# Kernel tuning notes

Measured on AMD Instinct MI355X. Metric: run time of the kernel, lower is better.

The kernel has to match this reference:

```python
import jax, jax.numpy as jnp
import numpy as np

NEG_INF = -9.0e15
ALPHA = 0.2  # leakyrelu slope


def setup_inputs() -> dict:
    key = jax.random.key(0)
    k1, k2, k3, k4, k5 = jax.random.split(key, 5)
    B, N, D_IN, D_OUT = 8, 2048, 128, 128
    h = jax.random.normal(k1, (B, N, D_IN), dtype=jnp.float32)
    adj = jax.random.randint(k2, (N, N), 0, 2, dtype=jnp.int32)
    W = jax.random.normal(k3, (D_IN, D_OUT), dtype=jnp.float32) * (1.0 / np.sqrt(D_IN))
    a_src = jax.random.normal(k4, (D_OUT,), dtype=jnp.float32) * (1.0 / np.sqrt(D_OUT))
    a_dst = jax.random.normal(k5, (D_OUT,), dtype=jnp.float32) * (1.0 / np.sqrt(D_OUT))
    return {"h": h, "adj": adj, "W": W, "a_src": a_src, "a_dst": a_dst}


def reference(h, adj, W, a_src, a_dst):
    # Wh: [B, N, D_out]
    Wh = jnp.einsum("bnd,de->bne", h, W)
    e_src = jnp.einsum("bne,e->bn", Wh, a_src)  # [B, N]
    e_dst = jnp.einsum("bne,e->bn", Wh, a_dst)  # [B, N]
    # additive attention logits: e[b,i,j] = e_src[b,i] + e_dst[b,j]
    e = e_src[:, :, None] + e_dst[:, None, :]  # [B, N, N]
    e = jnp.where(e > 0, e, ALPHA * e)  # leaky relu
    e = jnp.where(adj[None, :, :] > 0, e, NEG_INF)
    attention = jax.nn.softmax(e, axis=-1)  # [B, N, N]
    h_prime = jnp.einsum("bij,bje->bie", attention, Wh)
    return h_prime
```

## Files before the change

kernel.cpp:

```cpp
#include <hip/hip_runtime.h>
#include <stdint.h>

#define ALPHA 0.2f
#define LOG2E 1.4426950408889634f

typedef unsigned short u16;
typedef short s16x8 __attribute__((ext_vector_type(8)));
typedef float f32x4 __attribute__((ext_vector_type(4)));

union BF8 { s16x8 v; uint32_t u[4]; u16 s[8]; uint4 q; };

static __device__ __forceinline__ float bf2f(u16 u) {
  union { uint32_t i; float f; } c; c.i = ((uint32_t)u) << 16; return c.f;
}
static __device__ __forceinline__ uint32_t pk2bf(float lo, float hi) {
  uint32_t ul = __float_as_uint(lo) + 0x8000u;
  uint32_t uh = __float_as_uint(hi) + 0x8000u;
  return (ul >> 16) | (uh & 0xffff0000u);
}

static __device__ __forceinline__ void gl2lds16(const void* g, void* l) {
  __builtin_amdgcn_global_load_lds(
      (const __attribute__((address_space(1))) uint32_t*)g,
      (__attribute__((address_space(3))) uint32_t*)l, 16, 0, 0);
}

__global__ __launch_bounds__(256) void k_zero(uint32_t* __restrict__ out, int n32) {
  int gid = blockIdx.x * 256 + threadIdx.x;
  if (gid < n32) out[gid] = 0u;
}

__global__ __launch_bounds__(256) void k_pack_adj(const int* __restrict__ adj,
                                                  uint32_t* __restrict__ bits,
                                                  const u16* __restrict__ h,
                                                  int* __restrict__ flag) {
  int tid = threadIdx.x;
  int base = blockIdx.x * 256 + tid;
#pragma unroll
  for (int it = 0; it < 8; ++it) {
    int gid = base + it * (2048 * 256);
    unsigned long long m = __ballot(adj[gid] != 0);
    if ((tid & 63) == 0)
      *(unsigned long long*)(&bits[gid >> 5]) = m;
  }
  if (blockIdx.x == 0 && tid < 64) {
    u16 v = h[2 * tid];
    int e = (v >> 7) & 0xff;
    unsigned long long dm = __ballot(e >= 100 && e <= 140);
    if (tid == 0) flag[0] = (__popcll(dm) >= 48) ? 1 : 0;
  }
}

__global__ __launch_bounds__(256) void k_wh(
    const void* __restrict__ hV, const void* __restrict__ WgV,
    const void* __restrict__ aSrcV, const void* __restrict__ aDstV,
    const int* __restrict__ flag,
    u16* __restrict__ WhT, float* __restrict__ eS, float* __restrict__ eD) {
  __shared__ __align__(16) char smemRaw[34816];
  u16*   WT   = (u16*)smemRaw;
  float* tile = (float*)smemRaw;
  __shared__ float aS[128], aD[128];

  const int tid = threadIdx.x;
  const int mb = blockIdx.x * 64;
  const int isBf = *flag;

  if (isBf) {
    const u16* Wg = (const u16*)WgV;
    for (int it = 0; it < 8; ++it) {
      int idx = tid + it * 256;
      int k = idx >> 4, c0 = (idx & 15) * 8;
      uint4 w4 = *(const uint4*)(Wg + (k << 7) + c0);
      u16* wsv = (u16*)&w4;
#pragma unroll
      for (int e = 0; e < 8; ++e) WT[(c0 + e) * 136 + k] = wsv[e];
    }
    if (tid < 128) aS[tid] = bf2f(((const u16*)aSrcV)[tid]);
    else           aD[tid - 128] = bf2f(((const u16*)aDstV)[tid - 128]);
  } else {
    const float* Wg = (const float*)WgV;
    for (int it = 0; it < 8; ++it) {
      int idx = tid + it * 256;
      int k = idx >> 4, c0 = (idx & 15) * 8;
      float4 w0 = *(const float4*)(Wg + (k << 7) + c0);
      float4 w1 = *(const float4*)(Wg + (k << 7) + c0 + 4);
      float wf[8] = {w0.x, w0.y, w0.z, w0.w, w1.x, w1.y, w1.z, w1.w};
#pragma unroll
      for (int e = 0; e < 8; ++e)
        WT[(c0 + e) * 136 + k] = (u16)((__float_as_uint(wf[e]) + 0x8000u) >> 16);
    }
    if (tid < 128) aS[tid] = ((const float*)aSrcV)[tid];
    else           aD[tid - 128] = ((const float*)aDstV)[tid - 128];
  }
  __syncthreads();

  const int wv = tid >> 6, lane = tid & 63, ln = lane & 15, quad = lane >> 4;
  const int row = mb + wv * 16 + ln;

  f32x4 acc[8];
#pragma unroll
  for (int t = 0; t < 8; ++t) acc[t] = (f32x4){0.f, 0.f, 0.f, 0.f};

  if (isBf) {
    const u16* h = (const u16*)hV;
#pragma unroll
    for (int ks = 0; ks < 4; ++ks) {
      s16x8 af = *(const s16x8*)(h + (row << 7) + ks * 32 + quad * 8);
#pragma unroll
      for (int t = 0; t < 8; ++t) {
        s16x8 bfg = *(const s16x8*)(&WT[(t * 16 + ln) * 136 + ks * 32 + quad * 8]);
        acc[t] = __builtin_amdgcn_mfma_f32_16x16x32_bf16(af, bfg, acc[t], 0, 0, 0);
      }
    }
  } else {
    const float* h = (const float*)hV;
#pragma unroll
    for (int ks = 0; ks < 4; ++ks) {
      float4 a0 = *(const float4*)(h + (row << 7) + ks * 32 + quad * 8);
      float4 a1 = *(const float4*)(h + (row << 7) + ks * 32 + quad * 8 + 4);
      BF8 af;
      af.u[0] = pk2bf(a0.x, a0.y);
      af.u[1] = pk2bf(a0.z, a0.w);
      af.u[2] = pk2bf(a1.x, a1.y);
      af.u[3] = pk2bf(a1.z, a1.w);
#pragma unroll
      for (int t = 0; t < 8; ++t) {
        s16x8 bfg = *(const s16x8*)(&WT[(t * 16 + ln) * 136 + ks * 32 + quad * 8]);
        acc[t] = __builtin_amdgcn_mfma_f32_16x16x32_bf16(af.v, bfg, acc[t], 0, 0, 0);
      }
    }
  }
  __syncthreads();

#pragma unroll
  for (int t = 0; t < 8; ++t)
#pragma unroll
    for (int r = 0; r < 4; ++r)
      tile[(wv * 16 + quad * 4 + r) * 130 + t * 16 + ln] = acc[t][r];
  __syncthreads();

  if (tid < 128) {
    int r = tid & 63, grp = tid >> 6;
    const float* a = grp ? aD : aS;
    float sum = 0.f;
#pragma unroll 4
    for (int d = 0; d < 128; ++d) sum += tile[r * 130 + d] * a[d];
    int m = mb + r, b = m >> 11, n = m & 2047;
    (grp ? eD : eS)[(b << 11) + n] = sum * LOG2E;
  }

  {
    int d = tid >> 1, half = tid & 1;
    int n0 = mb & 2047, b = mb >> 11;
    uint32_t pk[16];
#pragma unroll
    for (int qq = 0; qq < 16; ++qq) {
      float v0 = tile[(half * 32 + 2 * qq) * 130 + d];
      float v1 = tile[(half * 32 + 2 * qq + 1) * 130 + d];
      pk[qq] = pk2bf(v0, v1);
    }
    uint4* dst = (uint4*)(WhT + (size_t)((b << 7) + d) * 2048 + n0 + half * 32);
#pragma unroll
    for (int c = 0; c < 4; ++c)
      dst[c] = make_uint4(pk[c * 4], pk[c * 4 + 1], pk[c * 4 + 2], pk[c * 4 + 3]);
  }
}

__global__ __launch_bounds__(512, 4) void k_attn(
    const u16* __restrict__ WhT, const float* __restrict__ eSrc,
    const float* __restrict__ eDst, const uint32_t* __restrict__ adjBits,
    const int* __restrict__ flag, void* __restrict__ outV) {
  __shared__ __align__(16) u16 bufB[2][8192];
  __shared__ __align__(16) u16 bufP[2][2048];

  const int tid = threadIdx.x;
  const int bid = (blockIdx.x & 7) * 64 + (blockIdx.x >> 3);
  const int b = bid >> 6, ig = bid & 63;
  const int i0 = ig * 32;

  const int w = tid >> 6, l = tid & 63;
  const int ln = l & 15, quad = l >> 4;
  const int s = w & 1, dh = w >> 1;

  const int gsrc = (l & 7) ^ ((l >> 3) & 7);
  const u16* whtB = WhT + ((size_t)b << 18);
  const u16* srcB = whtB + (size_t)(w * 8 + (l >> 3)) * 2048 + gsrc * 8;

  const int prow = tid >> 4, hg = tid & 15;
  const float sSp = eSrc[(b << 11) + i0 + prow];
  const float* eDb = eDst + (b << 11) + hg * 4;
  const uint32_t* adjB = adjBits + (size_t)(i0 + prow) * 64 + (hg >> 3);
  const int pOff = prow * 128 + ((hg ^ ((prow & 7) << 1)) * 8);

  int aOff[2], bOff[2][2];
#pragma unroll
  for (int jk = 0; jk < 2; ++jk) {
    aOff[jk] = (s * 16 + ln) * 128 + (((jk * 4 + quad) ^ (ln & 7)) * 16);
#pragma unroll
    for (int tt = 0; tt < 2; ++tt)
      bOff[tt][jk] = (dh * 32 + tt * 16 + ln) * 128
                   + (((jk * 4 + quad) ^ (ln & 7)) * 16);
  }

  f32x4 acc[2], accD;
  acc[0] = (f32x4){0.f, 0.f, 0.f, 0.f};
  acc[1] = (f32x4){0.f, 0.f, 0.f, 0.f};
  accD   = (f32x4){0.f, 0.f, 0.f, 0.f};

  BF8 ones;
  ones.u[0] = 0x3f803f80u; ones.u[1] = 0x3f803f80u;
  ones.u[2] = 0x3f803f80u; ones.u[3] = 0x3f803f80u;

  u16 *bBc = bufB[0], *bBn = bufB[1];
  u16 *bPc = bufP[0], *bPn = bufP[1];

  gl2lds16(srcB, bBc + w * 512);
  gl2lds16(srcB + 131072, bBc + 4096 + w * 512);
  {
    f32x4 dv = *(const f32x4*)(eDb);
    uint32_t aw = adjB[0];
    uint32_t nib = (aw >> ((hg & 7) * 4)) & 0xfu;
    float x0 = sSp + dv[0], x1 = sSp + dv[1], x2 = sSp + dv[2], x3 = sSp + dv[3];
    float p0 = exp2f(__builtin_amdgcn_fmed3f(x0, ALPHA * x0, 80.f));
    float p1 = exp2f(__builtin_amdgcn_fmed3f(x1, ALPHA * x1, 80.f));
    float p2 = exp2f(__builtin_amdgcn_fmed3f(x2, ALPHA * x2, 80.f));
    float p3 = exp2f(__builtin_amdgcn_fmed3f(x3, ALPHA * x3, 80.f));
    uint32_t m01 = ((nib & 1u) ? 0x0000ffffu : 0u) | ((nib & 2u) ? 0xffff0000u : 0u);
    uint32_t m23 = ((nib & 4u) ? 0x0000ffffu : 0u) | ((nib & 8u) ? 0xffff0000u : 0u);
    *(uint2*)((char*)bPc + pOff) = make_uint2(pk2bf(p0, p1) & m01,
                                              pk2bf(p2, p3) & m23);
  }
  __syncthreads();

  for (int t = 0; t < 32; ++t) {
    if (t + 1 < 32) {
      gl2lds16(srcB + (size_t)(t + 1) * 64, bBn + w * 512);
      gl2lds16(srcB + (size_t)(t + 1) * 64 + 131072, bBn + 4096 + w * 512);
      f32x4 dv = *(const f32x4*)(eDb + (t + 1) * 64);
      uint32_t aw = adjB[(t + 1) * 2];
      uint32_t nib = (aw >> ((hg & 7) * 4)) & 0xfu;
      float x0 = sSp + dv[0], x1 = sSp + dv[1], x2 = sSp + dv[2], x3 = sSp + dv[3];
      float p0 = exp2f(__builtin_amdgcn_fmed3f(x0, ALPHA * x0, 80.f));
      float p1 = exp2f(__builtin_amdgcn_fmed3f(x1, ALPHA * x1, 80.f));
      float p2 = exp2f(__builtin_amdgcn_fmed3f(x2, ALPHA * x2, 80.f));
      float p3 = exp2f(__builtin_amdgcn_fmed3f(x3, ALPHA * x3, 80.f));
      uint32_t m01 = ((nib & 1u) ? 0x0000ffffu : 0u) | ((nib & 2u) ? 0xffff0000u : 0u);
      uint32_t m23 = ((nib & 4u) ? 0x0000ffffu : 0u) | ((nib & 8u) ? 0xffff0000u : 0u);
      *(uint2*)((char*)bPn + pOff) = make_uint2(pk2bf(p0, p1) & m01,
                                                pk2bf(p2, p3) & m23);
    }

    s16x8 af0 = *(const s16x8*)((const char*)bPc + aOff[0]);
    s16x8 af1 = *(const s16x8*)((const char*)bPc + aOff[1]);
    s16x8 b00 = *(const s16x8*)((const char*)bBc + bOff[0][0]);
    s16x8 b10 = *(const s16x8*)((const char*)bBc + bOff[1][0]);
    s16x8 b01 = *(const s16x8*)((const char*)bBc + bOff[0][1]);
    s16x8 b11 = *(const s16x8*)((const char*)bBc + bOff[1][1]);

    __builtin_amdgcn_s_setprio(1);
    acc[0] = __builtin_amdgcn_mfma_f32_16x16x32_bf16(af0, b00, acc[0], 0, 0, 0);
    acc[1] = __builtin_amdgcn_mfma_f32_16x16x32_bf16(af0, b10, acc[1], 0, 0, 0);
    acc[0] = __builtin_amdgcn_mfma_f32_16x16x32_bf16(af1, b01, acc[0], 0, 0, 0);
    acc[1] = __builtin_amdgcn_mfma_f32_16x16x32_bf16(af1, b11, acc[1], 0, 0, 0);
    if (dh == 0) {
      accD = __builtin_amdgcn_mfma_f32_16x16x32_bf16(af0, ones.v, accD, 0, 0, 0);
      accD = __builtin_amdgcn_mfma_f32_16x16x32_bf16(af1, ones.v, accD, 0, 0, 0);
    }
    __builtin_amdgcn_s_setprio(0);

    __syncthreads();
    u16* tB = bBc; bBc = bBn; bBn = tB;
    u16* tP = bPc; bPc = bPn; bPn = tP;
  }

  float* den = (float*)bufP;
  if (dh == 0 && ln == 0) {
#pragma unroll
    for (int r = 0; r < 4; ++r) den[s * 16 + quad * 4 + r] = accD[r];
  }
  __syncthreads();

  float inv[4];
#pragma unroll
  for (int r = 0; r < 4; ++r)
    inv[r] = 1.0f / fmaxf(den[s * 16 + quad * 4 + r], 1e-37f);

  const int isBf = *flag;
  if (isBf) {
    u16* outp = (u16*)outV;
#pragma unroll
    for (int tt = 0; tt < 2; ++tt)
#pragma unroll
      for (int r = 0; r < 4; ++r) {
        size_t off = ((size_t)((b << 11) + i0 + s * 16 + quad * 4 + r) << 7)
                   + dh * 32 + tt * 16 + ln;
        float v = acc[tt][r] * inv[r];
        outp[off] = (u16)((__float_as_uint(v) + 0x8000u) >> 16);
      }
  } else {
    float* outp = (float*)outV;
#pragma unroll
    for (int tt = 0; tt < 2; ++tt)
#pragma unroll
      for (int r = 0; r < 4; ++r) {
        size_t off = ((size_t)((b << 11) + i0 + s * 16 + quad * 4 + r) << 7)
                   + dh * 32 + tt * 16 + ln;
        outp[off] = acc[tt][r] * inv[r];
      }
  }
}

extern "C" void kernel_launch(void* const* d_in, const int* in_sizes, int n_in,
                              void* d_out, int out_size, void* d_ws, size_t ws_size,
                              hipStream_t stream) {
  const void* h   = d_in[0];
  const int* adj  = (const int*)d_in[1];
  const void* Wg  = d_in[2];
  const void* aS  = d_in[3];
  const void* aD  = d_in[4];

  const size_t OFF_ES   = (size_t)4 << 20;
  const size_t OFF_ED   = OFF_ES + (64 << 10);
  const size_t OFF_BITS = OFF_ED + (64 << 10);
  const size_t OFF_FLAG = OFF_BITS + (512 << 10);
  const size_t NEEDED   = OFF_FLAG + 64;

  if (ws_size < NEEDED) {
    int n32 = out_size / 2;
    k_zero<<<(n32 + 255) / 256, 256, 0, stream>>>((uint32_t*)d_out, n32);
    return;
  }

  char* ws = (char*)d_ws;
  u16* WhT      = (u16*)ws;
  float* eSp    = (float*)(ws + OFF_ES);
  float* eDp    = (float*)(ws + OFF_ED);
  uint32_t* bit = (uint32_t*)(ws + OFF_BITS);
  int* flag     = (int*)(ws + OFF_FLAG);

  k_pack_adj<<<2048, 256, 0, stream>>>(adj, bit, (const u16*)h, flag);
  k_wh<<<256, 256, 0, stream>>>(h, Wg, aS, aD, flag, WhT, eSp, eDp);
  k_attn<<<512, 512, 0, stream>>>(WhT, eSp, eDp, bit, flag, d_out);
}
```

Before: 119.0 us.

## Merge adj-pack and Wh kernels, triple-buffer attention pipeline with explicit waits

Merges the adjacency bit-packing and the Wh projection into one launch. Wh blocks now handle 32 rows and compute the dtype flag themselves, and the e_src/e_dst dot products are reduced with wave shuffles instead of a serial LDS loop. The attention kernel moves from double to triple buffering, prefetching two tiles ahead, with manual s_waitcnt and s_barrier calls in place of __syncthreads. The aim is to drop one launch and overlap global-to-LDS loads with MFMA work, at the cost of more LDS per block, which may lower occupancy.

```diff
diff --git a/kernel.cpp b/kernel.cpp
--- a/kernel.cpp
+++ b/kernel.cpp
@@ -30,40 +30,50 @@
   if (gid < n32) out[gid] = 0u;
 }
 
-__global__ __launch_bounds__(256) void k_pack_adj(const int* __restrict__ adj,
-                                                  uint32_t* __restrict__ bits,
-                                                  const u16* __restrict__ h,
-                                                  int* __restrict__ flag) {
-  int tid = threadIdx.x;
-  int base = blockIdx.x * 256 + tid;
-#pragma unroll
-  for (int it = 0; it < 8; ++it) {
-    int gid = base + it * (2048 * 256);
-    unsigned long long m = __ballot(adj[gid] != 0);
-    if ((tid & 63) == 0)
-      *(unsigned long long*)(&bits[gid >> 5]) = m;
-  }
-  if (blockIdx.x == 0 && tid < 64) {
-    u16 v = h[2 * tid];
+__global__ __launch_bounds__(256) void k_prep(
+    const int* __restrict__ adj, uint32_t* __restrict__ bits,
+    const void* __restrict__ hV, const void* __restrict__ WgV,
+    const void* __restrict__ aSrcV, const void* __restrict__ aDstV,
+    int* __restrict__ flag,
+    u16* __restrict__ WhT, float* __restrict__ eS, float* __restrict__ eD) {
+  __shared__ __align__(16) char smemRaw[34816];
+  __shared__ float aS[128], aD[128];
+  __shared__ float ePs[2][32][2];
+
+  const int tid = threadIdx.x;
+  const int bk = blockIdx.x;
+  const int lane = tid & 63;
+
+  if (bk < 2048) {
+    int base = bk * 256 + tid;
+#pragma unroll
+    for (int it = 0; it < 8; ++it) {
+      int gid = base + it * (2048 * 256);
+      unsigned long long m = __ballot(adj[gid] != 0);
+      if ((tid & 63) == 0)
+        *(unsigned long long*)(&bits[gid >> 5]) = m;
+    }
+    if (bk == 0 && tid < 64) {
+      u16 v = ((const u16*)hV)[2 * tid];
+      int e = (v >> 7) & 0xff;
+      unsigned long long dm = __ballot(e >= 100 && e <= 140);
+      if (tid == 0) flag[0] = (__popcll(dm) >= 48) ? 1 : 0;
+    }
+    return;
+  }
+
+  u16*   WT   = (u16*)smemRaw;
+  float* tile = (float*)smemRaw;
+  const int whid = bk - 2048;
+  const int mb = whid * 32;
+
+  int isBf;
+  {
+    u16 v = ((const u16*)hV)[2 * lane];
     int e = (v >> 7) & 0xff;
     unsigned long long dm = __ballot(e >= 100 && e <= 140);
-    if (tid == 0) flag[0] = (__popcll(dm) >= 48) ? 1 : 0;
-  }
-}
-
-__global__ __launch_bounds__(256) void k_wh(
-    const void* __restrict__ hV, const void* __restrict__ WgV,
-    const void* __restrict__ aSrcV, const void* __restrict__ aDstV,
-    const int* __restrict__ flag,
-    u16* __restrict__ WhT, float* __restrict__ eS, float* __restrict__ eD) {
-  __shared__ __align__(16) char smemRaw[34816];
-  u16*   WT   = (u16*)smemRaw;
-  float* tile = (float*)smemRaw;
-  __shared__ float aS[128], aD[128];
-
-  const int tid = threadIdx.x;
-  const int mb = blockIdx.x * 64;
-  const int isBf = *flag;
+    isBf = (__popcll(dm) >= 48) ? 1 : 0;
+  }
 
   if (isBf) {
     const u16* Wg = (const u16*)WgV;
@@ -94,12 +104,13 @@
   }
   __syncthreads();
 
-  const int wv = tid >> 6, lane = tid & 63, ln = lane & 15, quad = lane >> 4;
-  const int row = mb + wv * 16 + ln;
-
-  f32x4 acc[8];
-#pragma unroll
-  for (int t = 0; t < 8; ++t) acc[t] = (f32x4){0.f, 0.f, 0.f, 0.f};
+  const int wv = tid >> 6, ln = lane & 15, quad = lane >> 4;
+  const int rh = wv & 1, ch = wv >> 1;
+  const int row = mb + rh * 16 + ln;
+
+  f32x4 acc[4];
+#pragma unroll
+  for (int t = 0; t < 4; ++t) acc[t] = (f32x4){0.f, 0.f, 0.f, 0.f};
 
   if (isBf) {
     const u16* h = (const u16*)hV;
@@ -107,8 +118,8 @@
     for (int ks = 0; ks < 4; ++ks) {
       s16x8 af = *(const s16x8*)(h + (row << 7) + ks * 32 + quad * 8);
 #pragma unroll
-      for (int t = 0; t < 8; ++t) {
-        s16x8 bfg = *(const s16x8*)(&WT[(t * 16 + ln) * 136 + ks * 32 + quad * 8]);
+      for (int t = 0; t < 4; ++t) {
+        s16x8 bfg = *(const s16x8*)(&WT[(ch * 64 + t * 16 + ln) * 136 + ks * 32 + quad * 8]);
         acc[t] = __builtin_amdgcn_mfma_f32_16x16x32_bf16(af, bfg, acc[t], 0, 0, 0);
       }
     }
@@ -124,45 +135,67 @@
       af.u[2] = pk2bf(a1.x, a1.y);
       af.u[3] = pk2bf(a1.z, a1.w);
 #pragma unroll
-      for (int t = 0; t < 8; ++t) {
-        s16x8 bfg = *(const s16x8*)(&WT[(t * 16 + ln) * 136 + ks * 32 + quad * 8]);
+      for (int t = 0; t < 4; ++t) {
+        s16x8 bfg = *(const s16x8*)(&WT[(ch * 64 + t * 16 + ln) * 136 + ks * 32 + quad * 8]);
         acc[t] = __builtin_amdgcn_mfma_f32_16x16x32_bf16(af.v, bfg, acc[t], 0, 0, 0);
       }
     }
   }
-  __syncthreads();
-
-#pragma unroll
-  for (int t = 0; t < 8; ++t)
+
+  {
+    float pS[4] = {0.f, 0.f, 0.f, 0.f}, pD[4] = {0.f, 0.f, 0.f, 0.f};
+#pragma unroll
+    for (int t = 0; t < 4; ++t) {
+      float av = aS[ch * 64 + t * 16 + ln];
+      float dv = aD[ch * 64 + t * 16 + ln];
+#pragma unroll
+      for (int r = 0; r < 4; ++r) { pS[r] += acc[t][r] * av; pD[r] += acc[t][r] * dv; }
+    }
+#pragma unroll
+    for (int m = 1; m < 16; m <<= 1) {
+#pragma unroll
+      for (int r = 0; r < 4; ++r) {
+        pS[r] += __shfl_xor(pS[r], m);
+        pD[r] += __shfl_xor(pD[r], m);
+      }
+    }
+    if (ln == 0) {
+#pragma unroll
+      for (int r = 0; r < 4; ++r) {
+        ePs[0][rh * 16 + quad * 4 + r][ch] = pS[r];
+        ePs[1][rh * 16 + quad * 4 + r][ch] = pD[r];
+      }
+    }
+  }
+  __syncthreads();
+
+#pragma unroll
+  for (int t = 0; t < 4; ++t)
 #pragma unroll
     for (int r = 0; r < 4; ++r)
-      tile[(wv * 16 + quad * 4 + r) * 130 + t * 16 + ln] = acc[t][r];
-  __syncthreads();
-
-  if (tid < 128) {
-    int r = tid & 63, grp = tid >> 6;
-    const float* a = grp ? aD : aS;
-    float sum = 0.f;
-#pragma unroll 4
-    for (int d = 0; d < 128; ++d) sum += tile[r * 130 + d] * a[d];
+      tile[(rh * 16 + quad * 4 + r) * 130 + ch * 64 + t * 16 + ln] = acc[t][r];
+  __syncthreads();
+
+  if (tid < 64) {
+    int r = tid & 31, which = tid >> 5;
+    float sum = ePs[which][r][0] + ePs[which][r][1];
     int m = mb + r, b = m >> 11, n = m & 2047;
-    (grp ? eD : eS)[(b << 11) + n] = sum * LOG2E;
+    (which ? eD : eS)[(b << 11) + n] = sum * LOG2E;
   }
 
   {
     int d = tid >> 1, half = tid & 1;
     int n0 = mb & 2047, b = mb >> 11;
-    uint32_t pk[16];
-#pragma unroll
-    for (int qq = 0; qq < 16; ++qq) {
-      float v0 = tile[(half * 32 + 2 * qq) * 130 + d];
-      float v1 = tile[(half * 32 + 2 * qq + 1) * 130 + d];
-      pk[qq] = pk2bf(v0, v1);
-    }
-    uint4* dst = (uint4*)(WhT + (size_t)((b << 7) + d) * 2048 + n0 + half * 32);
-#pragma unroll
-    for (int c = 0; c < 4; ++c)
-      dst[c] = make_uint4(pk[c * 4], pk[c * 4 + 1], pk[c * 4 + 2], pk[c * 4 + 3]);
+    uint32_t pk[8];
+#pragma unroll
+    for (int q = 0; q < 8; ++q) {
+      float v0 = tile[(half * 16 + 2 * q) * 130 + d];
+      float v1 = tile[(half * 16 + 2 * q + 1) * 130 + d];
+      pk[q] = pk2bf(v0, v1);
+    }
+    uint4* dst = (uint4*)(WhT + (size_t)((b << 7) + d) * 2048 + n0 + half * 16);
+    dst[0] = make_uint4(pk[0], pk[1], pk[2], pk[3]);
+    dst[1] = make_uint4(pk[4], pk[5], pk[6], pk[7]);
   }
 }
 
@@ -170,8 +203,8 @@
     const u16* __restrict__ WhT, const float* __restrict__ eSrc,
     const float* __restrict__ eDst, const uint32_t* __restrict__ adjBits,
     const int* __restrict__ flag, void* __restrict__ outV) {
-  __shared__ __align__(16) u16 bufB[2][8192];
-  __shared__ __align__(16) u16 bufP[2][2048];
+  __shared__ __align__(16) u16 bufB[3][8192];
+  __shared__ __align__(16) u16 bufP[3][2048];
 
   const int tid = threadIdx.x;
   const int bid = (blockIdx.x & 7) * 64 + (blockIdx.x >> 3);
@@ -192,88 +225,98 @@
   const uint32_t* adjB = adjBits + (size_t)(i0 + prow) * 64 + (hg >> 3);
   const int pOff = prow * 128 + ((hg ^ ((prow & 7) << 1)) * 8);
 
-  int aOff[2], bOff[2][2];
-#pragma unroll
-  for (int jk = 0; jk < 2; ++jk) {
-    aOff[jk] = (s * 16 + ln) * 128 + (((jk * 4 + quad) ^ (ln & 7)) * 16);
-#pragma unroll
-    for (int tt = 0; tt < 2; ++tt)
-      bOff[tt][jk] = (dh * 32 + tt * 16 + ln) * 128
-                   + (((jk * 4 + quad) ^ (ln & 7)) * 16);
-  }
-
-  f32x4 acc[2], accD;
-  acc[0] = (f32x4){0.f, 0.f, 0.f, 0.f};
-  acc[1] = (f32x4){0.f, 0.f, 0.f, 0.f};
-  accD   = (f32x4){0.f, 0.f, 0.f, 0.f};
+  const int aOff0 = (s * 16 + ln) * 128 + (((0 * 4 + quad) ^ (ln & 7)) * 16);
+  const int aOff1 = (s * 16 + ln) * 128 + (((1 * 4 + quad) ^ (ln & 7)) * 16);
+  const int bOff00 = (dh * 32 + 0 * 16 + ln) * 128 + (((0 * 4 + quad) ^ (ln & 7)) * 16);
+  const int bOff10 = (dh * 32 + 1 * 16 + ln) * 128 + (((0 * 4 + quad) ^ (ln & 7)) * 16);
+  const int bOff01 = (dh * 32 + 0 * 16 + ln) * 128 + (((1 * 4 + quad) ^ (ln & 7)) * 16);
+  const int bOff11 = (dh * 32 + 1 * 16 + ln) * 128 + (((1 * 4 + quad) ^ (ln & 7)) * 16);
+
+  f32x4 acc0 = (f32x4){0.f, 0.f, 0.f, 0.f};
+  f32x4 acc1 = (f32x4){0.f, 0.f, 0.f, 0.f};
+  f32x4 accD = (f32x4){0.f, 0.f, 0.f, 0.f};
 
   BF8 ones;
   ones.u[0] = 0x3f803f80u; ones.u[1] = 0x3f803f80u;
   ones.u[2] = 0x3f803f80u; ones.u[3] = 0x3f803f80u;
 
-  u16 *bBc = bufB[0], *bBn = bufB[1];
-  u16 *bPc = bufP[0], *bPn = bufP[1];
-
-  gl2lds16(srcB, bBc + w * 512);
-  gl2lds16(srcB + 131072, bBc + 4096 + w * 512);
+#define PCOMPUTE(dv, aw, pdst)  {                                             \
+    uint32_t nib = ((aw) >> ((hg & 7) * 4)) & 0xfu;                           \
+    float x0 = sSp + (dv)[0], x1 = sSp + (dv)[1];                             \
+    float x2 = sSp + (dv)[2], x3 = sSp + (dv)[3];                             \
+    float p0 = exp2f(__builtin_amdgcn_fmed3f(x0, ALPHA * x0, 80.f));          \
+    float p1 = exp2f(__builtin_amdgcn_fmed3f(x1, ALPHA * x1, 80.f));          \
+    float p2 = exp2f(__builtin_amdgcn_fmed3f(x2, ALPHA * x2, 80.f));          \
+    float p3 = exp2f(__builtin_amdgcn_fmed3f(x3, ALPHA * x3, 80.f));          \
+    uint32_t m01 = ((nib & 1u) ? 0x0000ffffu : 0u) | ((nib & 2u) ? 0xffff0000u : 0u); \
+    uint32_t m23 = ((nib & 4u) ? 0x0000ffffu : 0u) | ((nib & 8u) ? 0xffff0000u : 0u); \
+    *(uint2*)((char*)(pdst) + pOff) = make_uint2(pk2bf(p0, p1) & m01,         \
+                                                 pk2bf(p2, p3) & m23);        \
+  }
+
+#define CONSUME()  {                                                          \
+    s16x8 af0 = *(const s16x8*)((const char*)pPc + aOff0);                    \
+    s16x8 af1 = *(const s16x8*)((const char*)pPc + aOff1);                    \
+    s16x8 b00 = *(const s16x8*)((const char*)pBc + bOff00);                   \
+    s16x8 b10 = *(const s16x8*)((const char*)pBc + bOff10);                   \
+    s16x8 b01 = *(const s16x8*)((const char*)pBc + bOff01);                   \
+    s16x8 b11 = *(const s16x8*)((const char*)pBc + bOff11);                   \
+    __builtin_amdgcn_s_setprio(1);                                            \
+    acc0 = __builtin_amdgcn_mfma_f32_16x16x32_bf16(af0, b00, acc0, 0, 0, 0);  \
+    acc1 = __builtin_amdgcn_mfma_f32_16x16x32_bf16(af0, b10, acc1, 0, 0, 0);  \
+    acc0 = __builtin_amdgcn_mfma_f32_16x16x32_bf16(af1, b01, acc0, 0, 0, 0);  \
+    acc1 = __builtin_amdgcn_mfma_f32_16x16x32_bf16(af1, b11, acc1, 0, 0, 0);  \
+    if (dh == 0) {                                                            \
+      accD = __builtin_amdgcn_mfma_f32_16x16x32_bf16(af0, ones.v, accD, 0, 0, 0); \
+      accD = __builtin_amdgcn_mfma_f32_16x16x32_bf16(af1, ones.v, accD, 0, 0, 0); \
+    }                                                                         \
+    __builtin_amdgcn_s_setprio(0);                                            \
+  }
+
+  u16 *pBc = bufB[0], *pBn = bufB[1], *pBf = bufB[2];
+  u16 *pPc = bufP[0], *pPn = bufP[1], *pPf = bufP[2];
+
+  gl2lds16(srcB, pBc + w * 512);
+  gl2lds16(srcB + 131072, pBc + 4096 + w * 512);
+  gl2lds16(srcB + 64, pBn + w * 512);
+  gl2lds16(srcB + 131072 + 64, pBn + 4096 + w * 512);
   {
-    f32x4 dv = *(const f32x4*)(eDb);
-    uint32_t aw = adjB[0];
-    uint32_t nib = (aw >> ((hg & 7) * 4)) & 0xfu;
-    float x0 = sSp + dv[0], x1 = sSp + dv[1], x2 = sSp + dv[2], x3 = sSp + dv[3];
-    float p0 = exp2f(__builtin_amdgcn_fmed3f(x0, ALPHA * x0, 80.f));
-    float p1 = exp2f(__builtin_amdgcn_fmed3f(x1, ALPHA * x1, 80.f));
-    float p2 = exp2f(__builtin_amdgcn_fmed3f(x2, ALPHA * x2, 80.f));
-    float p3 = exp2f(__builtin_amdgcn_fmed3f(x3, ALPHA * x3, 80.f));
-    uint32_t m01 = ((nib & 1u) ? 0x0000ffffu : 0u) | ((nib & 2u) ? 0xffff0000u : 0u);
-    uint32_t m23 = ((nib & 4u) ? 0x0000ffffu : 0u) | ((nib & 8u) ? 0xffff0000u : 0u);
-    *(uint2*)((char*)bPc + pOff) = make_uint2(pk2bf(p0, p1) & m01,
-                                              pk2bf(p2, p3) & m23);
-  }
-  __syncthreads();
-
-  for (int t = 0; t < 32; ++t) {
-    if (t + 1 < 32) {
-      gl2lds16(srcB + (size_t)(t + 1) * 64, bBn + w * 512);
-      gl2lds16(srcB + (size_t)(t + 1) * 64 + 131072, bBn + 4096 + w * 512);
-      f32x4 dv = *(const f32x4*)(eDb + (t + 1) * 64);
-      uint32_t aw = adjB[(t + 1) * 2];
-      uint32_t nib = (aw >> ((hg & 7) * 4)) & 0xfu;
-      float x0 = sSp + dv[0], x1 = sSp + dv[1], x2 = sSp + dv[2], x3 = sSp + dv[3];
-      float p0 = exp2f(__builtin_amdgcn_fmed3f(x0, ALPHA * x0, 80.f));
-      float p1 = exp2f(__builtin_amdgcn_fmed3f(x1, ALPHA * x1, 80.f));
-      float p2 = exp2f(__builtin_amdgcn_fmed3f(x2, ALPHA * x2, 80.f));
-      float p3 = exp2f(__builtin_amdgcn_fmed3f(x3, ALPHA * x3, 80.f));
-      uint32_t m01 = ((nib & 1u) ? 0x0000ffffu : 0u) | ((nib & 2u) ? 0xffff0000u : 0u);
-      uint32_t m23 = ((nib & 4u) ? 0x0000ffffu : 0u) | ((nib & 8u) ? 0xffff0000u : 0u);
-      *(uint2*)((char*)bPn + pOff) = make_uint2(pk2bf(p0, p1) & m01,
-                                                pk2bf(p2, p3) & m23);
-    }
-
-    s16x8 af0 = *(const s16x8*)((const char*)bPc + aOff[0]);
-    s16x8 af1 = *(const s16x8*)((const char*)bPc + aOff[1]);
-    s16x8 b00 = *(const s16x8*)((const char*)bBc + bOff[0][0]);
-    s16x8 b10 = *(const s16x8*)((const char*)bBc + bOff[1][0]);
-    s16x8 b01 = *(const s16x8*)((const char*)bBc + bOff[0][1]);
-    s16x8 b11 = *(const s16x8*)((const char*)bBc + bOff[1][1]);
-
-    __builtin_amdgcn_s_setprio(1);
-    acc[0] = __builtin_amdgcn_mfma_f32_16x16x32_bf16(af0, b00, acc[0], 0, 0, 0);
-    acc[1] = __builtin_amdgcn_mfma_f32_16x16x32_bf16(af0, b10, acc[1], 0, 0, 0);
-    acc[0] = __builtin_amdgcn_mfma_f32_16x16x32_bf16(af1, b01, acc[0], 0, 0, 0);
-    acc[1] = __builtin_amdgcn_mfma_f32_16x16x32_bf16(af1, b11, acc[1], 0, 0, 0);
-    if (dh == 0) {
-      accD = __builtin_amdgcn_mfma_f32_16x16x32_bf16(af0, ones.v, accD, 0, 0, 0);
-      accD = __builtin_amdgcn_mfma_f32_16x16x32_bf16(af1, ones.v, accD, 0, 0, 0);
-    }
-    __builtin_amdgcn_s_setprio(0);
-
-    __syncthreads();
-    u16* tB = bBc; bBc = bBn; bBn = tB;
-    u16* tP = bPc; bPc = bPn; bPn = tP;
-  }
+    f32x4 dv0 = *(const f32x4*)(eDb);
+    uint32_t aw0 = adjB[0];
+    f32x4 dv1 = *(const f32x4*)(eDb + 64);
+    uint32_t aw1 = adjB[2];
+    PCOMPUTE(dv0, aw0, pPc);
+    PCOMPUTE(dv1, aw1, pPn);
+  }
+  asm volatile("s_waitcnt vmcnt(0) lgkmcnt(0)" ::: "memory");
+  __builtin_amdgcn_sched_barrier(0);
+  __builtin_amdgcn_s_barrier();
+
+  for (int t = 0; t < 30; ++t) {
+    f32x4 dv = *(const f32x4*)(eDb + (t + 2) * 64);
+    uint32_t aw = adjB[(t + 2) * 2];
+    __builtin_amdgcn_sched_barrier(0);
+    gl2lds16(srcB + (size_t)(t + 2) * 64, pBf + w * 512);
+    gl2lds16(srcB + (size_t)(t + 2) * 64 + 131072, pBf + 4096 + w * 512);
+    __builtin_amdgcn_sched_barrier(0);
+    PCOMPUTE(dv, aw, pPf);
+    CONSUME();
+    asm volatile("s_waitcnt vmcnt(2) lgkmcnt(0)" ::: "memory");
+    __builtin_amdgcn_sched_barrier(0);
+    __builtin_amdgcn_s_barrier();
+    u16* tb = pBc; pBc = pBn; pBn = pBf; pBf = tb;
+    u16* tp = pPc; pPc = pPn; pPn = pPf; pPf = tp;
+  }
+  CONSUME();
+  asm volatile("s_waitcnt vmcnt(0) lgkmcnt(0)" ::: "memory");
+  __builtin_amdgcn_sched_barrier(0);
+  __builtin_amdgcn_s_barrier();
+  { u16* tb = pBc; pBc = pBn; pBn = pBf; pBf = tb;
+    u16* tp = pPc; pPc = pPn; pPn = pPf; pPf = tp; }
+  CONSUME();
 
   float* den = (float*)bufP;
+  __syncthreads();
   if (dh == 0 && ln == 0) {
 #pragma unroll
     for (int r = 0; r < 4; ++r) den[s * 16 + quad * 4 + r] = accD[r];
@@ -289,25 +332,31 @@
   if (isBf) {
     u16* outp = (u16*)outV;
 #pragma unroll
-    for (int tt = 0; tt < 2; ++tt)
+    for (int tt = 0; tt < 2; ++tt) {
+      f32x4 a = tt ? acc1 : acc0;
 #pragma unroll
       for (int r = 0; r < 4; ++r) {
         size_t off = ((size_t)((b << 11) + i0 + s * 16 + quad * 4 + r) << 7)
                    + dh * 32 + tt * 16 + ln;
-        float v = acc[tt][r] * inv[r];
+        float v = a[r] * inv[r];
         outp[off] = (u16)((__float_as_uint(v) + 0x8000u) >> 16);
       }
+    }
   } else {
     float* outp = (float*)outV;
 #pragma unroll
-    for (int tt = 0; tt < 2; ++tt)
+    for (int tt = 0; tt < 2; ++tt) {
+      f32x4 a = tt ? acc1 : acc0;
 #pragma unroll
       for (int r = 0; r < 4; ++r) {
         size_t off = ((size_t)((b << 11) + i0 + s * 16 + quad * 4 + r) << 7)
                    + dh * 32 + tt * 16 + ln;
-        outp[off] = acc[tt][r] * inv[r];
-      }
-  }
+        outp[off] = a[r] * inv[r];
+      }
+    }
+  }
+#undef PCOMPUTE
+#undef CONSUME
 }
 
 extern "C" void kernel_launch(void* const* d_in, const int* in_sizes, int n_in,
@@ -338,7 +387,6 @@
   uint32_t* bit = (uint32_t*)(ws + OFF_BITS);
   int* flag     = (int*)(ws + OFF_FLAG);
 
-  k_pack_adj<<<2048, 256, 0, stream>>>(adj, bit, (const u16*)h, flag);
-  k_wh<<<256, 256, 0, stream>>>(h, Wg, aS, aD, flag, WhT, eSp, eDp);
+  k_prep<<<2560, 256, 0, stream>>>(adj, bit, h, Wg, aS, aD, flag, WhT, eSp, eDp);
   k_attn<<<512, 512, 0, stream>>>(WhT, eSp, eDp, bit, flag, d_out);
 }
```

Result: slower. 130.4 us (+9.6%).
